# Kernel optimization log

Hardware: AMD Instinct MI355X
Metric: run time of the kernel (lower is better)

Reference implementation:

```python
import jax, jax.numpy as jnp
import numpy as np

NUM_NODES = 200000
NUM_EDGES = 1250000
DIM = 64
K_LAYERS = 3
BATCH = 4096
CAND = 101  # 1 positive + 100 negatives


def setup_inputs() -> dict:
    key = jax.random.key(0)
    k1, k2, k3 = jax.random.split(key, 3)
    emb = jax.random.normal(k1, (NUM_NODES, DIM), dtype=jnp.float32)
    edge_index = jax.random.randint(k2, (2, NUM_EDGES), 0, NUM_NODES)
    batch = jax.random.randint(k3, (BATCH, CAND, 3), 0, NUM_NODES)
    return {"emb": emb, "edge_index": edge_index, "batch": batch,
            "num_nodes": NUM_NODES}


def reference(emb, edge_index, batch, num_nodes):
    # --- LightGCN.get_embedding: K rounds of symmetric-normalized SpMM ---
    row, col = edge_index[0], edge_index[1]  # source -> target
    ones = jnp.ones(row.shape[0], dtype=emb.dtype)
    deg = jax.ops.segment_sum(ones, col, num_segments=num_nodes)  # in-degree
    deg_safe = jnp.where(deg > 0, deg, 1.0)
    dis = jnp.where(deg > 0, jax.lax.rsqrt(deg_safe), 0.0)  # deg^{-1/2}, inf->0
    norm = dis[row] * dis[col]  # [E]

    alpha = 1.0 / (K_LAYERS + 1)  # uniform layer combination
    x = emb
    out = x * alpha
    for _ in range(K_LAYERS):
        # propagate: out[i] = sum_{(j->i)} norm_e * x[j]
        x = jax.ops.segment_sum(x[row] * norm[:, None], col,
                                num_segments=num_nodes)
        out = out + x * alpha

    # --- scoring: gather user/item embeddings, elementwise dot ---
    user_idx = batch[:, :, 0].reshape(-1)
    item_idx = batch[:, :, 1].reshape(-1)
    logits = jnp.sum(out[user_idx] * out[item_idx], axis=-1)  # [B*CAND]
    return logits.reshape(batch.shape[0], -1)
```

## Files before the change

kernel.cpp:

```cpp
#include <hip/hip_runtime.h>

#define DIM 64
#define BSHIFT 8
#define MAXNB 1024
#define CHUNK 4096

__device__ inline unsigned packbf(float a, float b) {
    unsigned ua = __float_as_uint(a), ub = __float_as_uint(b);
    unsigned ra = (ua + 0x7FFFu + ((ua >> 16) & 1u)) >> 16;
    unsigned rb = (ub + 0x7FFFu + ((ub >> 16) & 1u)) >> 16;
    return ra | (rb << 16);
}
__device__ inline void unpackbf(unsigned u, float& lo, float& hi) {
    lo = __uint_as_float(u << 16);
    hi = __uint_as_float(u & 0xFFFF0000u);
}
__device__ inline void acc_row(const uint4 v, float* s) {
    float lo, hi;
    unpackbf(v.x, lo, hi); s[0] += lo; s[1] += hi;
    unpackbf(v.y, lo, hi); s[2] += lo; s[3] += hi;
    unpackbf(v.z, lo, hi); s[4] += lo; s[5] += hi;
    unpackbf(v.w, lo, hi); s[6] += lo; s[7] += hi;
}
__device__ inline void acc_row_m(const uint4 v, float m, float* s) {
    float lo, hi;
    unpackbf(v.x, lo, hi); s[0] = fmaf(m, lo, s[0]); s[1] = fmaf(m, hi, s[1]);
    unpackbf(v.y, lo, hi); s[2] = fmaf(m, lo, s[2]); s[3] = fmaf(m, hi, s[3]);
    unpackbf(v.z, lo, hi); s[4] = fmaf(m, lo, s[4]); s[5] = fmaf(m, hi, s[5]);
    unpackbf(v.w, lo, hi); s[6] = fmaf(m, lo, s[6]); s[7] = fmaf(m, hi, s[7]);
}

__global__ __launch_bounds__(256) void block_hist_kernel(
        const int* __restrict__ col, int* __restrict__ H, int E, int NB,
        int nblocks) {
    __shared__ int h[MAXNB];
    int tid = threadIdx.x;
    for (int k = tid; k < NB; k += 256) h[k] = 0;
    __syncthreads();
    int base = blockIdx.x * CHUNK;
    #pragma unroll
    for (int k = 0; k < CHUNK / 256; k++) {
        int e = base + tid + k * 256;
        if (e < E) atomicAdd(&h[col[e] >> BSHIFT], 1);
    }
    __syncthreads();
    for (int k = tid; k < NB; k += 256) H[(size_t)k * nblocks + blockIdx.x] = h[k];
}

__global__ void scan_tile_sum_kernel(const int* __restrict__ H,
                                     int* __restrict__ T, int M) {
    int tid = threadIdx.x;
    int base = blockIdx.x * 1024 + tid * 4;
    int s = 0;
    #pragma unroll
    for (int k = 0; k < 4; k++)
        if (base + k < M) s += H[base + k];
    __shared__ int lds[256];
    lds[tid] = s;
    __syncthreads();
    for (int off = 128; off > 0; off >>= 1) {
        if (tid < off) lds[tid] += lds[tid + off];
        __syncthreads();
    }
    if (tid == 0) T[blockIdx.x] = lds[0];
}

__global__ void scan_tile_offsets_kernel(int* __restrict__ T, int nt) {
    __shared__ int lds[256];
    int tid = threadIdx.x;
    int v = (tid < nt) ? T[tid] : 0;
    lds[tid] = v;
    __syncthreads();
    for (int off = 1; off < 256; off <<= 1) {
        int t = (tid >= off) ? lds[tid - off] : 0;
        __syncthreads();
        lds[tid] += t;
        __syncthreads();
    }
    if (tid < nt) T[tid] = lds[tid] - v;
}

__global__ void scan_final_kernel(const int* __restrict__ H,
                                  const int* __restrict__ T,
                                  int* __restrict__ S, int M) {
    int tid = threadIdx.x;
    int base = blockIdx.x * 1024 + tid * 4;
    int c[4];
    int local = 0;
    #pragma unroll
    for (int k = 0; k < 4; k++) {
        c[k] = (base + k < M) ? H[base + k] : 0;
        local += c[k];
    }
    __shared__ int lds[256];
    lds[tid] = local;
    __syncthreads();
    for (int off = 1; off < 256; off <<= 1) {
        int t = (tid >= off) ? lds[tid - off] : 0;
        __syncthreads();
        lds[tid] += t;
        __syncthreads();
    }
    int excl = lds[tid] - local + T[blockIdx.x];
    #pragma unroll
    for (int k = 0; k < 4; k++) {
        if (base + k < M) S[base + k] = excl;
        excl += c[k];
    }
}

__global__ void bbase_kernel(const int* __restrict__ S, int* __restrict__ bbase,
                             int NB, int nblocks, int E) {
    int k = blockIdx.x * blockDim.x + threadIdx.x;
    if (k < NB) bbase[k] = S[(size_t)k * nblocks];
    if (k == 0) bbase[NB] = E;
}

__global__ __launch_bounds__(256) void scatter_binned_kernel(
        const int* __restrict__ row, const int* __restrict__ col,
        const int* __restrict__ S, unsigned* __restrict__ pairs, int E,
        int NB, int nblocks) {
    __shared__ unsigned stage[CHUNK];
    __shared__ int gdst[CHUNK];
    __shared__ int hist[MAXNB];
    __shared__ int pfx[MAXNB];
    __shared__ int gbase[MAXNB];
    int tid = threadIdx.x;
    int bid = blockIdx.x;
    int base = bid * CHUNK;
    int nloc = min(CHUNK, E - base);

    for (int b = tid; b < NB; b += 256) hist[b] = 0;
    __syncthreads();

    unsigned vals[CHUNK / 256];
    int keys[CHUNK / 256];
    #pragma unroll
    for (int k = 0; k < CHUNK / 256; k++) {
        int e = base + tid + k * 256;
        if (e < E) {
            int d = col[e];
            int s = row[e];
            keys[k] = d >> BSHIFT;
            vals[k] = (unsigned)s | ((unsigned)(d & 255) << 24);
            atomicAdd(&hist[keys[k]], 1);
        } else {
            keys[k] = -1;
        }
    }
    __syncthreads();

    int b0 = tid * 4;
    int c4[4];
    int loc = 0;
    #pragma unroll
    for (int k = 0; k < 4; k++) {
        c4[k] = (b0 + k < NB) ? hist[b0 + k] : 0;
        loc += c4[k];
    }
    gbase[tid] = loc;
    __syncthreads();
    for (int off = 1; off < 256; off <<= 1) {
        int t = (tid >= off) ? gbase[tid - off] : 0;
        __syncthreads();
        gbase[tid] += t;
        __syncthreads();
    }
    int excl = gbase[tid] - loc;
    #pragma unroll
    for (int k = 0; k < 4; k++) {
        if (b0 + k < NB) pfx[b0 + k] = excl;
        excl += c4[k];
    }
    __syncthreads();

    for (int b = tid; b < NB; b += 256) {
        gbase[b] = S[(size_t)b * nblocks + bid];
        hist[b] = pfx[b];
    }
    __syncthreads();

    #pragma unroll
    for (int k = 0; k < CHUNK / 256; k++) {
        if (keys[k] >= 0) {
            int slot = atomicAdd(&hist[keys[k]], 1);
            stage[slot] = vals[k];
            gdst[slot] = gbase[keys[k]] + (slot - pfx[keys[k]]);
        }
    }
    __syncthreads();

    for (int s = tid; s < nloc; s += 256) pairs[gdst[s]] = stage[s];
}

__global__ void fine_fill_kernel(const unsigned* __restrict__ pairs,
                                 const int* __restrict__ bbase,
                                 int* __restrict__ row_ptr,
                                 int* __restrict__ csr_src, int N, int E) {
    __shared__ int cnt[256];
    __shared__ int cur[256];
    int b = blockIdx.x;
    int tid = threadIdx.x;
    int beg = bbase[b], end = bbase[b + 1];
    cnt[tid] = 0;
    __syncthreads();
    for (int j = beg + tid; j < end; j += 256)
        atomicAdd(&cnt[pairs[j] >> 24], 1);
    __syncthreads();
    int v = cnt[tid];
    for (int off = 1; off < 256; off <<= 1) {
        int t = (tid >= off) ? cnt[tid - off] : 0;
        __syncthreads();
        cnt[tid] += t;
        __syncthreads();
    }
    int excl = cnt[tid] - v;
    int node = (b << BSHIFT) + tid;
    if (node < N) row_ptr[node] = beg + excl;
    cur[tid] = beg + excl;
    __syncthreads();
    for (int j = beg + tid; j < end; j += 256) {
        unsigned p = pairs[j];
        int pos = atomicAdd(&cur[p >> 24], 1);
        csr_src[pos] = (int)(p & 0xFFFFFFu);
    }
    if (b == 0 && tid == 0) row_ptr[N] = E;
}

__global__ void prescale_kernel(const float4* __restrict__ emb4,
                                const int* __restrict__ row_ptr,
                                uint4* __restrict__ z4, int N) {
    int t = blockIdx.x * blockDim.x + threadIdx.x;
    int i = t >> 3;
    int gl = t & 7;
    if (i >= N) return;
    int deg = row_ptr[i + 1] - row_ptr[i];
    float wd = (deg > 0) ? rsqrtf((float)deg) : 0.0f;
    size_t eo = (size_t)i * 16 + gl * 2;
    float4 a = emb4[eo], b = emb4[eo + 1];
    uint4 z;
    z.x = packbf(a.x * wd, a.y * wd);
    z.y = packbf(a.z * wd, a.w * wd);
    z.z = packbf(b.x * wd, b.y * wd);
    z.w = packbf(b.z * wd, b.w * wd);
    z4[(size_t)i * 8 + gl] = z;
}

__device__ inline void row_gather_sum(const int* __restrict__ csr_src,
                                      const uint4* __restrict__ z4, int b,
                                      int e, int gl, float* s) {
    if (b >= e) return;
    int e1 = e - 1;
    int j = b;
    int i0 = csr_src[j];
    int i1 = csr_src[min(j + 1, e1)];
    int i2 = csr_src[min(j + 2, e1)];
    int i3 = csr_src[min(j + 3, e1)];
    while (j < e) {
        uint4 v0 = z4[(size_t)i0 * 8 + gl];
        uint4 v1 = z4[(size_t)i1 * 8 + gl];
        uint4 v2 = z4[(size_t)i2 * 8 + gl];
        uint4 v3 = z4[(size_t)i3 * 8 + gl];
        int jn = j + 4;
        if (jn < e) {
            i0 = csr_src[jn];
            i1 = csr_src[min(jn + 1, e1)];
            i2 = csr_src[min(jn + 2, e1)];
            i3 = csr_src[min(jn + 3, e1)];
        }
        float m1 = (j + 1 < e) ? 1.0f : 0.0f;
        float m2 = (j + 2 < e) ? 1.0f : 0.0f;
        float m3 = (j + 3 < e) ? 1.0f : 0.0f;
        acc_row(v0, s);
        acc_row_m(v1, m1, s);
        acc_row_m(v2, m2, s);
        acc_row_m(v3, m3, s);
        j = jn;
    }
}

__global__ void spmm_pull_kernel(const int* __restrict__ row_ptr,
                                 const int* __restrict__ csr_src,
                                 const uint4* __restrict__ z4,
                                 uint4* __restrict__ znext4, int N) {
    int t = blockIdx.x * blockDim.x + threadIdx.x;
    int i = t >> 3;
    int gl = t & 7;
    if (i >= N) return;
    int b = row_ptr[i], e = row_ptr[i + 1];
    float s[8] = {0, 0, 0, 0, 0, 0, 0, 0};
    row_gather_sum(csr_src, z4, b, e, gl, s);
    int deg = e - b;
    float wd = (deg > 0) ? rsqrtf((float)deg) : 0.0f;
    float w2 = wd * wd;
    uint4 z;
    z.x = packbf(s[0] * w2, s[1] * w2);
    z.y = packbf(s[2] * w2, s[3] * w2);
    z.z = packbf(s[4] * w2, s[5] * w2);
    z.w = packbf(s[6] * w2, s[7] * w2);
    znext4[(size_t)i * 8 + gl] = z;
}

__global__ void spmm_combine_kernel(const int* __restrict__ row_ptr,
                                    const int* __restrict__ csr_src,
                                    const uint4* __restrict__ z2,
                                    const uint4* __restrict__ z1,
                                    const float4* __restrict__ emb4,
                                    uint4* __restrict__ accb, int N) {
    int t = blockIdx.x * blockDim.x + threadIdx.x;
    int i = t >> 3;
    int gl = t & 7;
    if (i >= N) return;
    int b = row_ptr[i], e = row_ptr[i + 1];
    float s[8] = {0, 0, 0, 0, 0, 0, 0, 0};
    row_gather_sum(csr_src, z2, b, e, gl, s);
    int deg = e - b;
    float wd = (deg > 0) ? rsqrtf((float)deg) : 0.0f;
    float sq = (deg > 0) ? sqrtf((float)deg) : 0.0f;
    size_t zo = (size_t)i * 8 + gl;
    uint4 a1 = z1[zo], a2 = z2[zo];
    float w[8] = {0, 0, 0, 0, 0, 0, 0, 0};
    acc_row(a1, w); acc_row(a2, w);
    size_t eo = (size_t)i * 16 + gl * 2;
    float4 e0 = emb4[eo], e1 = emb4[eo + 1];
    float r0 = e0.x + sq * w[0] + wd * s[0];
    float r1 = e0.y + sq * w[1] + wd * s[1];
    float r2 = e0.z + sq * w[2] + wd * s[2];
    float r3 = e0.w + sq * w[3] + wd * s[3];
    float r4 = e1.x + sq * w[4] + wd * s[4];
    float r5 = e1.y + sq * w[5] + wd * s[5];
    float r6 = e1.z + sq * w[6] + wd * s[6];
    float r7 = e1.w + sq * w[7] + wd * s[7];
    uint4 z;
    z.x = packbf(r0, r1);
    z.y = packbf(r2, r3);
    z.z = packbf(r4, r5);
    z.w = packbf(r6, r7);
    accb[zo] = z;
}

__global__ void score_kernel(const int* __restrict__ batch,
                             const uint4* __restrict__ accb,
                             float* __restrict__ out, int P) {
    int t = blockIdx.x * blockDim.x + threadIdx.x;
    int p = t >> 3;
    int gl = t & 7;
    if (p >= P) return;
    int u = batch[(size_t)p * 3 + 0];
    int it = batch[(size_t)p * 3 + 1];
    uint4 a = accb[(size_t)u * 8 + gl];
    uint4 b = accb[(size_t)it * 8 + gl];
    float sa[8] = {0, 0, 0, 0, 0, 0, 0, 0};
    float sb[8] = {0, 0, 0, 0, 0, 0, 0, 0};
    acc_row(a, sa);
    acc_row(b, sb);
    float s = sa[0] * sb[0] + sa[1] * sb[1] + sa[2] * sb[2] + sa[3] * sb[3] +
              sa[4] * sb[4] + sa[5] * sb[5] + sa[6] * sb[6] + sa[7] * sb[7];
    s += __shfl_xor(s, 4, 64);
    s += __shfl_xor(s, 2, 64);
    s += __shfl_xor(s, 1, 64);
    if (gl == 0) out[p] = s * 0.0625f;
}

extern "C" void kernel_launch(void* const* d_in, const int* in_sizes, int n_in,
                              void* d_out, int out_size, void* d_ws,
                              size_t ws_size, hipStream_t stream) {
    const float* emb = (const float*)d_in[0];
    const int* edge_index = (const int*)d_in[1];
    const int* batch = (const int*)d_in[2];
    float* out = (float*)d_out;

    const int N = in_sizes[0] / DIM;
    const int E = in_sizes[1] / 2;
    const int P = out_size;
    const int NB = (N + 255) >> BSHIFT;
    const int nblocks = (E + CHUNK - 1) / CHUNK;
    const int M = NB * nblocks;
    const int nt = (M + 1023) / 1024;

    const int* row = edge_index;
    const int* col = edge_index + E;

    const size_t zbytes = (size_t)N * DIM * 2;

    auto align256 = [](size_t x) { return (x + 255) & ~(size_t)255; };
    char* ws = (char*)d_ws;
    uint4* z0   = (uint4*)ws; ws += align256(zbytes);
    uint4* z1   = (uint4*)ws; ws += align256(zbytes);
    uint4* z2   = (uint4*)ws; ws += align256(zbytes);
    uint4* accb = (uint4*)ws; ws += align256(zbytes);
    unsigned* pairs = (unsigned*)ws; ws += align256((size_t)E * 4);
    int* csr_src    = (int*)ws;      ws += align256((size_t)E * 4);
    int* row_ptr    = (int*)ws;      ws += align256((size_t)(N + 1) * 4);
    int* H          = (int*)ws;      ws += align256((size_t)M * 4);
    int* S          = (int*)ws;      ws += align256((size_t)M * 4);
    int* T          = (int*)ws;      ws += align256(256 * 4);
    int* bbase      = (int*)ws;

    block_hist_kernel<<<nblocks, 256, 0, stream>>>(col, H, E, NB, nblocks);
    scan_tile_sum_kernel<<<nt, 256, 0, stream>>>(H, T, M);
    scan_tile_offsets_kernel<<<1, 256, 0, stream>>>(T, nt);
    scan_final_kernel<<<nt, 256, 0, stream>>>(H, T, S, M);
    bbase_kernel<<<(NB + 255) / 256, 256, 0, stream>>>(S, bbase, NB, nblocks, E);
    scatter_binned_kernel<<<nblocks, 256, 0, stream>>>(row, col, S, pairs, E,
                                                       NB, nblocks);
    fine_fill_kernel<<<NB, 256, 0, stream>>>(pairs, bbase, row_ptr, csr_src,
                                             N, E);

    const int nodeBlocks = (N * 8 + 255) / 256;

    prescale_kernel<<<nodeBlocks, 256, 0, stream>>>((const float4*)emb,
                                                    row_ptr, z0, N);

    spmm_pull_kernel<<<nodeBlocks, 256, 0, stream>>>(row_ptr, csr_src, z0, z1, N);
    spmm_pull_kernel<<<nodeBlocks, 256, 0, stream>>>(row_ptr, csr_src, z1, z2, N);
    spmm_combine_kernel<<<nodeBlocks, 256, 0, stream>>>(row_ptr, csr_src, z2,
                                                        z1, (const float4*)emb,
                                                        accb, N);

    score_kernel<<<(P * 8 + 255) / 256, 256, 0, stream>>>(batch, accb, out, P);
}
```

Baseline: 251.7 us.

## Fuse prescale into first SpMM, merge bbase into scan, halve binning chunk

Removes the prescale kernel. The first propagation layer now gathers the fp32 embeddings directly and multiplies each by a per-node deg^-1/2 weight, which fine_fill computes. The bbase kernel is folded into scan_final, which now scans 8 elements per thread. The binning CHUNK drops to 2048 so more blocks run, at the cost of a larger histogram matrix. The first SpMM reads fp32 rows, twice the bytes of bf16 rows, in exchange for skipping one full write and re-read of the bf16 z0 buffer and one launch.

```diff
diff --git a/kernel.cpp b/kernel.cpp
--- a/kernel.cpp
+++ b/kernel.cpp
@@ -3,7 +3,8 @@
 #define DIM 64
 #define BSHIFT 8
 #define MAXNB 1024
-#define CHUNK 4096
+#define CHUNK 2048
+#define EPT (CHUNK / 256)
 
 __device__ inline unsigned packbf(float a, float b) {
     unsigned ua = __float_as_uint(a), ub = __float_as_uint(b);
@@ -39,7 +40,7 @@
     __syncthreads();
     int base = blockIdx.x * CHUNK;
     #pragma unroll
-    for (int k = 0; k < CHUNK / 256; k++) {
+    for (int k = 0; k < EPT; k++) {
         int e = base + tid + k * 256;
         if (e < E) atomicAdd(&h[col[e] >> BSHIFT], 1);
     }
@@ -50,10 +51,10 @@
 __global__ void scan_tile_sum_kernel(const int* __restrict__ H,
                                      int* __restrict__ T, int M) {
     int tid = threadIdx.x;
-    int base = blockIdx.x * 1024 + tid * 4;
+    int base = blockIdx.x * 2048 + tid * 8;
     int s = 0;
     #pragma unroll
-    for (int k = 0; k < 4; k++)
+    for (int k = 0; k < 8; k++)
         if (base + k < M) s += H[base + k];
     __shared__ int lds[256];
     lds[tid] = s;
@@ -82,13 +83,15 @@
 
 __global__ void scan_final_kernel(const int* __restrict__ H,
                                   const int* __restrict__ T,
-                                  int* __restrict__ S, int M) {
-    int tid = threadIdx.x;
-    int base = blockIdx.x * 1024 + tid * 4;
-    int c[4];
+                                  int* __restrict__ S,
+                                  int* __restrict__ bbase, int M, int nblocks,
+                                  int NB, int E) {
+    int tid = threadIdx.x;
+    int base = blockIdx.x * 2048 + tid * 8;
+    int c[8];
     int local = 0;
     #pragma unroll
-    for (int k = 0; k < 4; k++) {
+    for (int k = 0; k < 8; k++) {
         c[k] = (base + k < M) ? H[base + k] : 0;
         local += c[k];
     }
@@ -103,17 +106,15 @@
     }
     int excl = lds[tid] - local + T[blockIdx.x];
     #pragma unroll
-    for (int k = 0; k < 4; k++) {
-        if (base + k < M) S[base + k] = excl;
+    for (int k = 0; k < 8; k++) {
+        int idx = base + k;
+        if (idx < M) {
+            S[idx] = excl;
+            if (idx - (idx / nblocks) * nblocks == 0) bbase[idx / nblocks] = excl;
+        }
         excl += c[k];
     }
-}
-
-__global__ void bbase_kernel(const int* __restrict__ S, int* __restrict__ bbase,
-                             int NB, int nblocks, int E) {
-    int k = blockIdx.x * blockDim.x + threadIdx.x;
-    if (k < NB) bbase[k] = S[(size_t)k * nblocks];
-    if (k == 0) bbase[NB] = E;
+    if (blockIdx.x == 0 && tid == 0) bbase[NB] = E;
 }
 
 __global__ __launch_bounds__(256) void scatter_binned_kernel(
@@ -133,10 +134,10 @@
     for (int b = tid; b < NB; b += 256) hist[b] = 0;
     __syncthreads();
 
-    unsigned vals[CHUNK / 256];
-    int keys[CHUNK / 256];
-    #pragma unroll
-    for (int k = 0; k < CHUNK / 256; k++) {
+    unsigned vals[EPT];
+    int keys[EPT];
+    #pragma unroll
+    for (int k = 0; k < EPT; k++) {
         int e = base + tid + k * 256;
         if (e < E) {
             int d = col[e];
@@ -181,7 +182,7 @@
     __syncthreads();
 
     #pragma unroll
-    for (int k = 0; k < CHUNK / 256; k++) {
+    for (int k = 0; k < EPT; k++) {
         if (keys[k] >= 0) {
             int slot = atomicAdd(&hist[keys[k]], 1);
             stage[slot] = vals[k];
@@ -196,6 +197,7 @@
 __global__ void fine_fill_kernel(const unsigned* __restrict__ pairs,
                                  const int* __restrict__ bbase,
                                  int* __restrict__ row_ptr,
+                                 float* __restrict__ wdv,
                                  int* __restrict__ csr_src, int N, int E) {
     __shared__ int cnt[256];
     __shared__ int cur[256];
@@ -216,7 +218,10 @@
     }
     int excl = cnt[tid] - v;
     int node = (b << BSHIFT) + tid;
-    if (node < N) row_ptr[node] = beg + excl;
+    if (node < N) {
+        row_ptr[node] = beg + excl;
+        wdv[node] = (v > 0) ? rsqrtf((float)v) : 0.0f;
+    }
     cur[tid] = beg + excl;
     __syncthreads();
     for (int j = beg + tid; j < end; j += 256) {
@@ -225,25 +230,6 @@
         csr_src[pos] = (int)(p & 0xFFFFFFu);
     }
     if (b == 0 && tid == 0) row_ptr[N] = E;
-}
-
-__global__ void prescale_kernel(const float4* __restrict__ emb4,
-                                const int* __restrict__ row_ptr,
-                                uint4* __restrict__ z4, int N) {
-    int t = blockIdx.x * blockDim.x + threadIdx.x;
-    int i = t >> 3;
-    int gl = t & 7;
-    if (i >= N) return;
-    int deg = row_ptr[i + 1] - row_ptr[i];
-    float wd = (deg > 0) ? rsqrtf((float)deg) : 0.0f;
-    size_t eo = (size_t)i * 16 + gl * 2;
-    float4 a = emb4[eo], b = emb4[eo + 1];
-    uint4 z;
-    z.x = packbf(a.x * wd, a.y * wd);
-    z.y = packbf(a.z * wd, a.w * wd);
-    z.z = packbf(b.x * wd, b.y * wd);
-    z.w = packbf(b.z * wd, b.w * wd);
-    z4[(size_t)i * 8 + gl] = z;
 }
 
 __device__ inline void row_gather_sum(const int* __restrict__ csr_src,
@@ -279,10 +265,79 @@
     }
 }
 
-__global__ void spmm_pull_kernel(const int* __restrict__ row_ptr,
-                                 const int* __restrict__ csr_src,
-                                 const uint4* __restrict__ z4,
-                                 uint4* __restrict__ znext4, int N) {
+__global__ __launch_bounds__(256) void spmm_first_kernel(
+        const int* __restrict__ row_ptr, const int* __restrict__ csr_src,
+        const float* __restrict__ wdv, const float4* __restrict__ emb4,
+        uint4* __restrict__ z1, int N) {
+    int t = blockIdx.x * blockDim.x + threadIdx.x;
+    int i = t >> 3;
+    int gl = t & 7;
+    if (i >= N) return;
+    int b = row_ptr[i], e = row_ptr[i + 1];
+    float s[8] = {0, 0, 0, 0, 0, 0, 0, 0};
+    if (b < e) {
+        int e1 = e - 1;
+        int j = b;
+        int i0 = csr_src[j];
+        int i1 = csr_src[min(j + 1, e1)];
+        int i2 = csr_src[min(j + 2, e1)];
+        int i3 = csr_src[min(j + 3, e1)];
+        while (j < e) {
+            float w0 = wdv[i0];
+            float w1 = wdv[i1];
+            float w2 = wdv[i2];
+            float w3 = wdv[i3];
+            size_t o0 = (size_t)i0 * 16 + gl * 2;
+            size_t o1 = (size_t)i1 * 16 + gl * 2;
+            size_t o2 = (size_t)i2 * 16 + gl * 2;
+            size_t o3 = (size_t)i3 * 16 + gl * 2;
+            float4 a0 = emb4[o0], c0 = emb4[o0 + 1];
+            float4 a1 = emb4[o1], c1 = emb4[o1 + 1];
+            float4 a2 = emb4[o2], c2 = emb4[o2 + 1];
+            float4 a3 = emb4[o3], c3 = emb4[o3 + 1];
+            int jn = j + 4;
+            if (jn < e) {
+                i0 = csr_src[jn];
+                i1 = csr_src[min(jn + 1, e1)];
+                i2 = csr_src[min(jn + 2, e1)];
+                i3 = csr_src[min(jn + 3, e1)];
+            }
+            w1 = (j + 1 < e) ? w1 : 0.0f;
+            w2 = (j + 2 < e) ? w2 : 0.0f;
+            w3 = (j + 3 < e) ? w3 : 0.0f;
+            s[0] = fmaf(w0, a0.x, s[0]); s[1] = fmaf(w0, a0.y, s[1]);
+            s[2] = fmaf(w0, a0.z, s[2]); s[3] = fmaf(w0, a0.w, s[3]);
+            s[4] = fmaf(w0, c0.x, s[4]); s[5] = fmaf(w0, c0.y, s[5]);
+            s[6] = fmaf(w0, c0.z, s[6]); s[7] = fmaf(w0, c0.w, s[7]);
+            s[0] = fmaf(w1, a1.x, s[0]); s[1] = fmaf(w1, a1.y, s[1]);
+            s[2] = fmaf(w1, a1.z, s[2]); s[3] = fmaf(w1, a1.w, s[3]);
+            s[4] = fmaf(w1, c1.x, s[4]); s[5] = fmaf(w1, c1.y, s[5]);
+            s[6] = fmaf(w1, c1.z, s[6]); s[7] = fmaf(w1, c1.w, s[7]);
+            s[0] = fmaf(w2, a2.x, s[0]); s[1] = fmaf(w2, a2.y, s[1]);
+            s[2] = fmaf(w2, a2.z, s[2]); s[3] = fmaf(w2, a2.w, s[3]);
+            s[4] = fmaf(w2, c2.x, s[4]); s[5] = fmaf(w2, c2.y, s[5]);
+            s[6] = fmaf(w2, c2.z, s[6]); s[7] = fmaf(w2, c2.w, s[7]);
+            s[0] = fmaf(w3, a3.x, s[0]); s[1] = fmaf(w3, a3.y, s[1]);
+            s[2] = fmaf(w3, a3.z, s[2]); s[3] = fmaf(w3, a3.w, s[3]);
+            s[4] = fmaf(w3, c3.x, s[4]); s[5] = fmaf(w3, c3.y, s[5]);
+            s[6] = fmaf(w3, c3.z, s[6]); s[7] = fmaf(w3, c3.w, s[7]);
+            j = jn;
+        }
+    }
+    int deg = e - b;
+    float wi = (deg > 0) ? rsqrtf((float)deg) : 0.0f;
+    float w2i = wi * wi;
+    uint4 z;
+    z.x = packbf(s[0] * w2i, s[1] * w2i);
+    z.y = packbf(s[2] * w2i, s[3] * w2i);
+    z.z = packbf(s[4] * w2i, s[5] * w2i);
+    z.w = packbf(s[6] * w2i, s[7] * w2i);
+    z1[(size_t)i * 8 + gl] = z;
+}
+
+__global__ __launch_bounds__(256) void spmm_pull_kernel(
+        const int* __restrict__ row_ptr, const int* __restrict__ csr_src,
+        const uint4* __restrict__ z4, uint4* __restrict__ znext4, int N) {
     int t = blockIdx.x * blockDim.x + threadIdx.x;
     int i = t >> 3;
     int gl = t & 7;
@@ -301,12 +356,10 @@
     znext4[(size_t)i * 8 + gl] = z;
 }
 
-__global__ void spmm_combine_kernel(const int* __restrict__ row_ptr,
-                                    const int* __restrict__ csr_src,
-                                    const uint4* __restrict__ z2,
-                                    const uint4* __restrict__ z1,
-                                    const float4* __restrict__ emb4,
-                                    uint4* __restrict__ accb, int N) {
+__global__ __launch_bounds__(256) void spmm_combine_kernel(
+        const int* __restrict__ row_ptr, const int* __restrict__ csr_src,
+        const uint4* __restrict__ z2, const uint4* __restrict__ z1,
+        const float4* __restrict__ emb4, uint4* __restrict__ accb, int N) {
     int t = blockIdx.x * blockDim.x + threadIdx.x;
     int i = t >> 3;
     int gl = t & 7;
@@ -339,9 +392,9 @@
     accb[zo] = z;
 }
 
-__global__ void score_kernel(const int* __restrict__ batch,
-                             const uint4* __restrict__ accb,
-                             float* __restrict__ out, int P) {
+__global__ __launch_bounds__(256) void score_kernel(
+        const int* __restrict__ batch, const uint4* __restrict__ accb,
+        float* __restrict__ out, int P) {
     int t = blockIdx.x * blockDim.x + threadIdx.x;
     int p = t >> 3;
     int gl = t & 7;
@@ -376,7 +429,7 @@
     const int NB = (N + 255) >> BSHIFT;
     const int nblocks = (E + CHUNK - 1) / CHUNK;
     const int M = NB * nblocks;
-    const int nt = (M + 1023) / 1024;
+    const int nt = (M + 2047) / 2048;
 
     const int* row = edge_index;
     const int* col = edge_index + E;
@@ -385,13 +438,13 @@
 
     auto align256 = [](size_t x) { return (x + 255) & ~(size_t)255; };
     char* ws = (char*)d_ws;
-    uint4* z0   = (uint4*)ws; ws += align256(zbytes);
     uint4* z1   = (uint4*)ws; ws += align256(zbytes);
     uint4* z2   = (uint4*)ws; ws += align256(zbytes);
     uint4* accb = (uint4*)ws; ws += align256(zbytes);
     unsigned* pairs = (unsigned*)ws; ws += align256((size_t)E * 4);
     int* csr_src    = (int*)ws;      ws += align256((size_t)E * 4);
     int* row_ptr    = (int*)ws;      ws += align256((size_t)(N + 1) * 4);
+    float* wdv      = (float*)ws;    ws += align256((size_t)N * 4);
     int* H          = (int*)ws;      ws += align256((size_t)M * 4);
     int* S          = (int*)ws;      ws += align256((size_t)M * 4);
     int* T          = (int*)ws;      ws += align256(256 * 4);
@@ -400,19 +453,16 @@
     block_hist_kernel<<<nblocks, 256, 0, stream>>>(col, H, E, NB, nblocks);
     scan_tile_sum_kernel<<<nt, 256, 0, stream>>>(H, T, M);
     scan_tile_offsets_kernel<<<1, 256, 0, stream>>>(T, nt);
-    scan_final_kernel<<<nt, 256, 0, stream>>>(H, T, S, M);
-    bbase_kernel<<<(NB + 255) / 256, 256, 0, stream>>>(S, bbase, NB, nblocks, E);
+    scan_final_kernel<<<nt, 256, 0, stream>>>(H, T, S, bbase, M, nblocks, NB, E);
     scatter_binned_kernel<<<nblocks, 256, 0, stream>>>(row, col, S, pairs, E,
                                                        NB, nblocks);
-    fine_fill_kernel<<<NB, 256, 0, stream>>>(pairs, bbase, row_ptr, csr_src,
-                                             N, E);
+    fine_fill_kernel<<<NB, 256, 0, stream>>>(pairs, bbase, row_ptr, wdv,
+                                             csr_src, N, E);
 
     const int nodeBlocks = (N * 8 + 255) / 256;
 
-    prescale_kernel<<<nodeBlocks, 256, 0, stream>>>((const float4*)emb,
-                                                    row_ptr, z0, N);
-
-    spmm_pull_kernel<<<nodeBlocks, 256, 0, stream>>>(row_ptr, csr_src, z0, z1, N);
+    spmm_first_kernel<<<nodeBlocks, 256, 0, stream>>>(row_ptr, csr_src, wdv,
+                                                      (const float4*)emb, z1, N);
     spmm_pull_kernel<<<nodeBlocks, 256, 0, stream>>>(row_ptr, csr_src, z1, z2, N);
     spmm_combine_kernel<<<nodeBlocks, 256, 0, stream>>>(row_ptr, csr_src, z2,
                                                         z1, (const float4*)emb,
```

Measured after the change: 262.8 us. 4.4% more time.
